# Performance work log

Hardware: AMD Instinct MI355X
Metric: run time of the kernel (lower is better)

## Reference

```python
import jax, jax.numpy as jnp
import numpy as np

IMG = 640.0  # square input image, strides 16/32 -> 40x40 and 20x20 grids

def _decode_level(raw, stride):
    # raw: [B, 5+C, H, W] -> [B, H*W, 5+C] with xy/wh decoded (get_output_and_grid)
    b, ch, h, w = raw.shape
    out = raw.transpose(0, 2, 3, 1).reshape(b, h * w, ch)
    yv, xv = jnp.meshgrid(jnp.arange(h), jnp.arange(w), indexing='ij')
    gx = xv.reshape(-1).astype(raw.dtype)
    gy = yv.reshape(-1).astype(raw.dtype)
    xy = (out[..., :2] + jnp.stack([gx, gy], -1)[None]) * stride
    wh = jnp.exp(out[..., 2:4]) * stride
    out = jnp.concatenate([xy, wh, out[..., 4:]], -1)
    return out, gx, gy, jnp.full((h * w,), stride, raw.dtype)

def _pairwise_iou(a, b):
    # a:[M,4], b:[A,4] in cxcywh -> [M,A] (bboxes_iou, xyxy=False)
    tl = jnp.maximum(a[:, None, :2] - a[:, None, 2:] * 0.5, b[None, :, :2] - b[None, :, 2:] * 0.5)
    br = jnp.minimum(a[:, None, :2] + a[:, None, 2:] * 0.5, b[None, :, :2] + b[None, :, 2:] * 0.5)
    inter = jnp.prod(br - tl, -1) * (tl < br).all(-1)
    area_a = a[:, 2] * a[:, 3]
    area_b = b[:, 2] * b[:, 3]
    return inter / (area_a[:, None] + area_b[None, :] - inter + 1e-16)

def _iou_loss(p, t):
    # YOLOX IOUloss (loss_type='iou'): 1 - iou^2, elementwise over [..., 4] cxcywh
    tl = jnp.maximum(p[..., :2] - p[..., 2:] * 0.5, t[..., :2] - t[..., 2:] * 0.5)
    br = jnp.minimum(p[..., :2] + p[..., 2:] * 0.5, t[..., :2] + t[..., 2:] * 0.5)
    inter = jnp.prod(br - tl, -1) * (tl < br).all(-1)
    iou = inter / (p[..., 2] * p[..., 3] + t[..., 2] * t[..., 3] - inter + 1e-16)
    return 1.0 - iou ** 2

def _bce_logits(x, t):
    # BCEWithLogitsLoss(reduction='none') = softplus(x) - x*t (stable)
    return jnp.logaddexp(0.0, x) - x * t

def _assign_one(bbox_p, cls_p, obj_p, gtb, gtc, gtv, ax, ay, st):
    # SimOTA assignment for one image (mask form of get_assignments, which is @no_grad).
    # bbox_p:[A,4] cls_p:[A,C] obj_p:[A] gtb:[M,4] px cxcywh, gtv:[M] valid mask.
    m = gtb.shape[0]
    axc = (ax + 0.5) * st
    ayc = (ay + 0.5) * st
    gl = gtb[:, 0] - 0.5 * gtb[:, 2]; gr = gtb[:, 0] + 0.5 * gtb[:, 2]
    gtp = gtb[:, 1] - 0.5 * gtb[:, 3]; gbt = gtb[:, 1] + 0.5 * gtb[:, 3]
    in_box = ((axc[None] > gl[:, None]) & (axc[None] < gr[:, None]) &
              (ayc[None] > gtp[:, None]) & (ayc[None] < gbt[:, None])) & gtv[:, None]
    r = 2.5  # center_radius
    in_ctr = ((axc[None] > gtb[:, 0:1] - r * st[None]) & (axc[None] < gtb[:, 0:1] + r * st[None]) &
              (ayc[None] > gtb[:, 1:2] - r * st[None]) & (ayc[None] < gtb[:, 1:2] + r * st[None])) & gtv[:, None]
    fg_cand = (in_box | in_ctr).any(0)          # candidate anchors (fg_mask pre-filter)
    in_both = in_box & in_ctr
    ious = _pairwise_iou(gtb, bbox_p)            # [M,A]
    p = jnp.sqrt(jax.nn.sigmoid(cls_p) * jax.nn.sigmoid(obj_p)[:, None])[None]  # [1,A,C]
    t = jax.nn.one_hot(gtc, cls_p.shape[-1], dtype=p.dtype)[:, None, :]          # [M,1,C]
    eps = 1e-12
    cls_cost = -(t * jnp.log(p + eps) + (1.0 - t) * jnp.log(1.0 - p + eps)).sum(-1)
    invalid = (~fg_cand)[None] | (~gtv)[:, None]
    cost = cls_cost - 3.0 * jnp.log(ious + 1e-8) + 1e5 * (~in_both) + 1e9 * invalid
    ious_m = jnp.where(invalid, 0.0, ious)
    topk, _ = jax.lax.top_k(ious_m, 10)
    dk = jnp.maximum(topk.sum(-1).astype(jnp.int32), 1)  # dynamic_k, clamp min=1
    dk = jnp.where(gtv, dk, 0)
    ranks = jnp.argsort(jnp.argsort(cost, axis=1), axis=1)
    matching = ranks < dk[:, None]                        # top dynamic_k lowest-cost anchors per gt
    conflict = matching.sum(0) > 1
    best_gt = jnp.argmin(cost, 0)
    matching = jnp.where(conflict[None], jnp.arange(m)[:, None] == best_gt[None], matching)
    fg = matching.any(0)
    matched = jnp.argmax(matching, 0).astype(jnp.int32)
    pred_iou = jnp.where(matching, ious, 0.0).sum(0)
    return fg, matched, pred_iou

def _forward(out_l0, out_l1, gt_boxes, gt_classes, num_gts):
    ncls = out_l0.shape[1] - 5
    decs, xs, ys, ss = [], [], [], []
    for raw, stride in ((out_l0, 16.0), (out_l1, 32.0)):
        d, gx, gy, s = _decode_level(raw, stride)
        decs.append(d); xs.append(gx); ys.append(gy); ss.append(s)
    outputs = jnp.concatenate(decs, 1)  # [B, A, 5+C]
    ax = jnp.concatenate(xs); ay = jnp.concatenate(ys); st = jnp.concatenate(ss)
    bbox_p = outputs[..., :4]; obj_p = outputs[..., 4]; cls_p = outputs[..., 5:]
    gtb = gt_boxes * IMG  # normalized -> pixels (imgs_w == imgs_h == IMG)
    gtv = jnp.arange(gt_boxes.shape[1])[None, :] < num_gts[:, None]
    sg = jax.lax.stop_gradient  # get_assignments runs under torch.no_grad
    fg, matched, pred_iou = jax.vmap(_assign_one, in_axes=(0, 0, 0, 0, 0, 0, None, None, None))(
        sg(bbox_p), sg(cls_p), sg(obj_p), sg(gtb), gt_classes, gtv, ax, ay, st)
    fgf = fg.astype(outputs.dtype)
    cls_t = jax.nn.one_hot(jnp.take_along_axis(gt_classes, matched, 1), ncls,
                           dtype=outputs.dtype) * pred_iou[..., None] * fgf[..., None]
    reg_t = jnp.take_along_axis(gtb, matched[..., None], 1)  # [B,A,4]
    num_fg = jnp.maximum(fgf.sum(), 1.0)
    loss_iou = (_iou_loss(bbox_p, reg_t) * fgf).sum() / num_fg
    loss_obj = _bce_logits(obj_p, fgf).sum() / num_fg
    loss_cls = (_bce_logits(cls_p, cls_t) * fgf[..., None]).sum() / num_fg
    total = 5.0 * loss_iou + loss_obj + loss_cls
    return (total, 5.0 * loss_iou, loss_obj, loss_cls,
            num_fg / jnp.maximum(num_gts.sum().astype(outputs.dtype), 1.0))

def setup_inputs() -> dict:
    key = jax.random.key(0)
    k1, k2, k3, k4, k5 = jax.random.split(key, 5)
    return {
        'out_l0': jax.random.normal(k1, (64, 25, 40, 40), jnp.float32),
        'out_l1': jax.random.normal(k2, (64, 25, 20, 20), jnp.float32),
        'gt_boxes': jax.random.uniform(k3, (64, 100, 4), jnp.float32, 1e-3, 1.0),
        'gt_classes': jax.random.randint(k4, (64, 100), 0, 20).astype(jnp.int32),
        'num_gts': jax.random.randint(k5, (64,), 0, 100).astype(jnp.int32),
    }

def reference(out_l0, out_l1, gt_boxes, gt_classes, num_gts):
    return _forward(out_l0, out_l1, gt_boxes, gt_classes, num_gts)
```

## Files before the change

### kernel.cpp

```cpp
#include <hip/hip_runtime.h>
#include <cfloat>
#include <climits>

#define NB 64
#define NA 2000
#define NAP 2048
#define NA0 1600
#define NC 20
#define NM 100

__device__ __forceinline__ void anchor_geom(int a, float& axc, float& ayc, float& st) {
    if (a < NA0) {
        st = 16.0f;
        int x = a % 40, y = a / 40;
        axc = ((float)x + 0.5f) * 16.0f;
        ayc = ((float)y + 0.5f) * 16.0f;
    } else {
        st = 32.0f;
        int aa = a - NA0;
        int x = aa % 20, y = aa / 20;
        axc = ((float)x + 0.5f) * 32.0f;
        ayc = ((float)y + 0.5f) * 32.0f;
    }
}

__device__ __forceinline__ float cost_row(const float4 g, float clsc, const float4 pe, float areaP,
                                          float axc, float ayc, float st, bool fc) {
    float glx = g.x - 0.5f * g.z, grx = g.x + 0.5f * g.z;
    float gty = g.y - 0.5f * g.w, gby = g.y + 0.5f * g.w;
    float tlx = fmaxf(glx, pe.x);
    float tly = fmaxf(gty, pe.z);
    float brx = fminf(grx, pe.y);
    float bry = fminf(gby, pe.w);
    float inter = (brx - tlx) * (bry - tly);
    bool ok = (tlx < brx) && (tly < bry);
    inter = ok ? inter : 0.0f;
    float iou = inter / ((g.z * g.w + areaP) - inter + 1e-16f);
    bool ib = (axc > glx) && (axc < grx) && (ayc > gty) && (ayc < gby);
    bool ic = (axc > g.x - 2.5f * st) && (axc < g.x + 2.5f * st)
           && (ayc > g.y - 2.5f * st) && (ayc < g.y + 2.5f * st);
    return ((clsc - 3.0f * __logf(iou + 1e-8f)) + ((ib && ic) ? 0.0f : 1e5f)) + (fc ? 0.0f : 1e9f);
}

__device__ __forceinline__ unsigned int wave_max_u32(unsigned int x) {
    unsigned int y;
    y = (unsigned)__builtin_amdgcn_update_dpp((int)x, (int)x, 0x111, 0xf, 0xf, false); x = max(x, y);
    y = (unsigned)__builtin_amdgcn_update_dpp((int)x, (int)x, 0x112, 0xf, 0xf, false); x = max(x, y);
    y = (unsigned)__builtin_amdgcn_update_dpp((int)x, (int)x, 0x114, 0xf, 0xf, false); x = max(x, y);
    y = (unsigned)__builtin_amdgcn_update_dpp((int)x, (int)x, 0x118, 0xf, 0xf, false); x = max(x, y);
    y = (unsigned)__builtin_amdgcn_update_dpp((int)x, (int)x, 0x142, 0xa, 0xf, false); x = max(x, y);
    y = (unsigned)__builtin_amdgcn_update_dpp((int)x, (int)x, 0x143, 0xc, 0xf, false); x = max(x, y);
    return (unsigned)__builtin_amdgcn_readlane((int)x, 63);
}
__device__ __forceinline__ unsigned int wave_min_u32(unsigned int x) {
    unsigned int y;
    y = (unsigned)__builtin_amdgcn_update_dpp((int)x, (int)x, 0x111, 0xf, 0xf, false); x = min(x, y);
    y = (unsigned)__builtin_amdgcn_update_dpp((int)x, (int)x, 0x112, 0xf, 0xf, false); x = min(x, y);
    y = (unsigned)__builtin_amdgcn_update_dpp((int)x, (int)x, 0x114, 0xf, 0xf, false); x = min(x, y);
    y = (unsigned)__builtin_amdgcn_update_dpp((int)x, (int)x, 0x118, 0xf, 0xf, false); x = min(x, y);
    y = (unsigned)__builtin_amdgcn_update_dpp((int)x, (int)x, 0x142, 0xa, 0xf, false); x = min(x, y);
    y = (unsigned)__builtin_amdgcn_update_dpp((int)x, (int)x, 0x143, 0xc, 0xf, false); x = min(x, y);
    return (unsigned)__builtin_amdgcn_readlane((int)x, 63);
}

__global__ __launch_bounds__(256) void k_decode(const float* __restrict__ l0, const float* __restrict__ l1,
                                                const float* __restrict__ gt_boxes, const int* __restrict__ num_gts,
                                                float4* __restrict__ ext, float* __restrict__ decA,
                                                float* __restrict__ qq,
                                                unsigned long long* __restrict__ fgw, unsigned int* __restrict__ cm,
                                                float* __restrict__ sp) {
    int b = blockIdx.y;
    int a = blockIdx.x * 256 + threadIdx.x;
    int lane = threadIdx.x & 63;
    __shared__ float4 sext[NM];
    __shared__ float2 sctr[NM];
    __shared__ int sng;
    if (threadIdx.x < NM) {
        float4 g = ((const float4*)gt_boxes)[b * NM + threadIdx.x];
        g.x *= 640.0f; g.y *= 640.0f; g.z *= 640.0f; g.w *= 640.0f;
        sext[threadIdx.x] = make_float4(g.x - 0.5f * g.z, g.x + 0.5f * g.z,
                                        g.y - 0.5f * g.w, g.y + 0.5f * g.w);
        sctr[threadIdx.x] = make_float2(g.x, g.y);
    }
    if (threadIdx.x == 0) sng = num_gts[b];
    __syncthreads();

    size_t pidx = (size_t)b * NAP + a;
    if (a >= NA) {
        cm[pidx] = 0;
        return;
    }

    float v[25];
    if (a < NA0) {
        const float* p = l0 + (size_t)b * 25 * NA0 + a;
#pragma unroll
        for (int c = 0; c < 25; c++) v[c] = p[(size_t)c * NA0];
    } else {
        const float* p = l1 + (size_t)b * 25 * 400 + (a - NA0);
#pragma unroll
        for (int c = 0; c < 25; c++) v[c] = p[(size_t)c * 400];
    }
    float axc, ayc, st;
    anchor_geom(a, axc, ayc, st);
    float gx, gy;
    if (a < NA0) { gx = (float)(a % 40); gy = (float)(a / 40); }
    else { int aa = a - NA0; gx = (float)(aa % 20); gy = (float)(aa / 20); }
    float4 pb;
    pb.x = (v[0] + gx) * st;
    pb.y = (v[1] + gy) * st;
    pb.z = expf(v[2]) * st;
    pb.w = expf(v[3]) * st;
    ext[pidx] = make_float4(pb.x - 0.5f * pb.z, pb.x + 0.5f * pb.z,
                            pb.y - 0.5f * pb.w, pb.y + 0.5f * pb.w);
    decA[pidx] = pb.z * pb.w;

    float sob = 1.0f / (1.0f + __expf(-v[4]));
    float d[NC];
    float s = 0.0f;
    float spv = 0.0f;
#pragma unroll
    for (int c = 0; c < NC; c++) {
        float x = v[5 + c];
        float sc = 1.0f / (1.0f + __expf(-x));
        float p = sqrtf(sc * sob);
        float lp = __logf(p + 1e-12f);
        float lq = __logf(1.0f - p + 1e-12f);
        s += -lq;
        d[c] = lq - lp;
        spv += fmaxf(x, 0.0f) + log1pf(__expf(-fabsf(x)));
    }
#pragma unroll
    for (int c = 0; c < NC; c++)
        qq[((size_t)b * NC + c) * NAP + a] = s + d[c];
    sp[pidx] = spv;

    int ng = sng;
    int f = 0;
    float rst = 2.5f * st;
    for (int m = 0; m < ng; m++) {
        float4 e = sext[m];
        float2 cc = sctr[m];
        bool ib = (axc > e.x) && (axc < e.y) && (ayc > e.z) && (ayc < e.w);
        bool ic = (axc > cc.x - rst) && (axc < cc.x + rst) && (ayc > cc.y - rst) && (ayc < cc.y + rst);
        if (ib || ic) { f = 1; break; }
    }
    unsigned long long mk = __ballot(f);
    if (lane == 0) fgw[(size_t)b * 32 + (a >> 6)] = mk;
    cm[pidx] = 0;
}

__global__ __launch_bounds__(256) void k_assign(const float* __restrict__ gt_boxes, const int* __restrict__ gt_classes,
                                                const int* __restrict__ num_gts, const float4* __restrict__ ext,
                                                const float* __restrict__ decA,
                                                const float* __restrict__ qq, const unsigned long long* __restrict__ fgw,
                                                unsigned int* __restrict__ cm) {
    int lane = threadIdx.x & 63;
    int wv = __builtin_amdgcn_readfirstlane((int)(threadIdx.x >> 6));
    int rloc = wv >> 1, half = wv & 1;
    int row = __builtin_amdgcn_readfirstlane((int)(blockIdx.x * 2 + rloc));
    int b = row / NM, m = row - b * NM;
    bool valid = (m < num_gts[b]);

    __shared__ unsigned int lA[2][2][10];
    __shared__ unsigned int lB[2][2][10];
    __shared__ unsigned int lmeta[2];
    __shared__ unsigned int lthr[2];

    unsigned int ik[16], ck[16];
    size_t bNA = (size_t)b * NAP;
    unsigned int inc = (1u << 20) + (unsigned)m;

    if (valid) {
        float4 g = ((const float4*)gt_boxes)[b * NM + m];
        g.x *= 640.0f; g.y *= 640.0f; g.z *= 640.0f; g.w *= 640.0f;
        int tc = gt_classes[b * NM + m];
        const float* qrow = qq + ((size_t)b * NC + tc) * NAP;

        float glx = g.x - 0.5f * g.z, grx = g.x + 0.5f * g.z;
        float gty = g.y - 0.5f * g.w, gby = g.y + 0.5f * g.w;
        float areag = g.z * g.w;
        float c16l = g.x - 40.0f, c16r = g.x + 40.0f, c16t = g.y - 40.0f, c16b = g.y + 40.0f;
        float c32l = g.x - 80.0f, c32r = g.x + 80.0f, c32t = g.y - 80.0f, c32b = g.y + 80.0f;

#pragma unroll
        for (int j = 0; j < 16; j++) {
            int jj = half * 16 + j;
            int a = jj * 64 + lane;
            bool lvl0 = jj < 25;
            float stj = lvl0 ? 16.0f : 32.0f;
            int rel = lvl0 ? a : (a - NA0);
            int W = lvl0 ? 40 : 20;
            int gyv = rel / W;
            int gxv = rel - gyv * W;
            float axc = ((float)gxv + 0.5f) * stj;
            float ayc = ((float)gyv + 0.5f) * stj;
            unsigned long long fw = fgw[(size_t)b * 32 + jj];
            bool fc = (fw >> lane) & 1ULL;
            float4 pe = ext[bNA + a];
            float areaP = decA[bNA + a];
            float clsc = qrow[a];
            float tlx = fmaxf(glx, pe.x);
            float tly = fmaxf(gty, pe.z);
            float brx = fminf(grx, pe.y);
            float bry = fminf(gby, pe.w);
            float inter = (brx - tlx) * (bry - tly);
            bool ok = (tlx < brx) && (tly < bry);
            inter = ok ? inter : 0.0f;
            float iou = inter / ((areag + areaP) - inter + 1e-16f);
            bool ib = (axc > glx) && (axc < grx) && (ayc > gty) && (ayc < gby);
            bool ic = lvl0 ? ((axc > c16l) && (axc < c16r) && (ayc > c16t) && (ayc < c16b))
                           : ((axc > c32l) && (axc < c32r) && (ayc > c32t) && (ayc < c32b));
            float cc = ((clsc - 3.0f * __logf(iou + 1e-8f)) + ((ib && ic) ? 0.0f : 1e5f)) + (fc ? 0.0f : 1e9f);
            float im = fc ? iou : 0.0f;
            ik[j] = (__float_as_uint(im) & 0xFFFFF800u) | (unsigned)a;
            ck[j] = (__float_as_uint(cc) & 0xFFFFF800u) | (unsigned)a;
        }

        int k = 0;
#pragma unroll 1
        for (; k < 10; ++k) {
            unsigned int t[8];
#pragma unroll
            for (int h = 0; h < 8; h++) t[h] = max(ik[2 * h], ik[2 * h + 1]);
#pragma unroll
            for (int w = 4; w >= 1; w >>= 1)
#pragma unroll
                for (int h = 0; h < w; h++) t[h] = max(t[h], t[h + w]);
            unsigned int mx = wave_max_u32(t[0]);
            if ((mx & 0xFFFFF800u) == 0u) break;
            if (lane == 0) lA[rloc][half][k] = mx;
#pragma unroll
            for (int j = 0; j < 16; j++) ik[j] = (ik[j] == mx) ? 0u : ik[j];
        }
#pragma unroll 1
        for (; k < 10; ++k) if (lane == 0) lA[rloc][half][k] = 0u;
    }
    __syncthreads();

    if (valid && half == 0 && lane == 0) {
        int i0 = 0, i1 = 0;
        float s = 0.0f;
        for (int k = 0; k < 10; k++) {
            unsigned int a0 = lA[rloc][0][i0], a1 = lA[rloc][1][i1];
            unsigned int mx;
            if (a1 > a0) { mx = a1; i1++; } else { mx = a0; i0++; }
            s += __uint_as_float(mx & 0xFFFFF800u);
        }
        int dk = (int)s;
        if (dk < 1) dk = 1;
        lmeta[rloc] = (unsigned)dk;
    }
    __syncthreads();

    int dkv = 0;
    if (valid) dkv = __builtin_amdgcn_readfirstlane((int)lmeta[rloc]);

    if (valid) {
#pragma unroll 1
        for (int k = 0; k < dkv; k++) {
            unsigned int t[8];
#pragma unroll
            for (int h = 0; h < 8; h++) t[h] = min(ck[2 * h], ck[2 * h + 1]);
#pragma unroll
            for (int w = 4; w >= 1; w >>= 1)
#pragma unroll
                for (int h = 0; h < w; h++) t[h] = min(t[h], t[h + w]);
            unsigned int mn = wave_min_u32(t[0]);
            if (lane == 0) lB[rloc][half][k] = mn;
#pragma unroll
            for (int j = 0; j < 16; j++) ck[j] = (ck[j] == mn) ? 0xFFFFFFFFu : ck[j];
        }
    }
    __syncthreads();

    if (valid && half == 0 && lane == 0) {
        int i0 = 0, i1 = 0;
        unsigned int thr = 0;
        for (int k = 0; k < dkv; k++) {
            unsigned int a0 = lB[rloc][0][i0], a1 = lB[rloc][1][i1];
            if (a1 < a0) { thr = a1; i1++; } else { thr = a0; i0++; }
        }
        lthr[rloc] = thr;
    }
    __syncthreads();

    if (valid) {
        unsigned int thr = (unsigned)__builtin_amdgcn_readfirstlane((int)lthr[rloc]);
        unsigned int mb = 0;
#pragma unroll
        for (int j = 0; j < 16; j++) if (ck[j] <= thr) mb |= 1u << j;
#pragma unroll 1
        for (int k = 0; k < dkv; k++) {
            unsigned int e = lB[rloc][half][k];
            if (e <= thr) {
                unsigned int idx = e & 0x7FFu;
                if ((int)(idx & 63u) == lane) mb |= 1u << ((int)(idx >> 6) - half * 16);
            }
        }
#pragma unroll
        for (int j = 0; j < 16; j++) {
            if ((mb >> j) & 1u) atomicAdd(&cm[bNA + (size_t)(half * 16 + j) * 64 + lane], inc);
        }
    }
}

__global__ __launch_bounds__(256) void k_resolve(const float* __restrict__ l0, const float* __restrict__ l1,
                                                 const float* __restrict__ gt_boxes, const int* __restrict__ gt_classes,
                                                 const int* __restrict__ num_gts,
                                                 const float4* __restrict__ ext, const float* __restrict__ decA,
                                                 const float* __restrict__ qq, const unsigned long long* __restrict__ fgw,
                                                 const unsigned int* __restrict__ cm,
                                                 const float* __restrict__ sp,
                                                 float* __restrict__ partials) {
    int gtid = blockIdx.x * 256 + threadIdx.x;
    int lane = threadIdx.x & 63;
    int b = gtid >> 11;
    int a = gtid & (NAP - 1);
    bool real = a < NA;

    unsigned int word = real ? cm[gtid] : 0u;
    int mres = (int)(word & 0xFFFFFu);

    unsigned long long msk = __ballot((word >> 20) >= 2u);
    if (msk != 0ull) {
        int base = gtid & ~63;
        int ng = num_gts[b];
        while (msk) {
            int t = __ffsll((long long)msk) - 1;
            msk &= msk - 1;
            int idx = base + t;
            int aa = idx & (NAP - 1);
            float4 pe = ext[idx];
            float areaP = decA[idx];
            float axc, ayc, st;
            anchor_geom(aa, axc, ayc, st);
            bool fcq = (fgw[(size_t)b * 32 + (aa >> 6)] >> (aa & 63)) & 1ULL;
            unsigned int best = 0xFFFFFFFFu;
#pragma unroll
            for (int half = 0; half < 2; half++) {
                int m = half * 64 + lane;
                if (m < ng) {
                    float4 g = ((const float4*)gt_boxes)[b * NM + m];
                    g.x *= 640.0f; g.y *= 640.0f; g.z *= 640.0f; g.w *= 640.0f;
                    int tcm = gt_classes[b * NM + m];
                    float clsc = qq[((size_t)b * NC + tcm) * NAP + aa];
                    float cc = cost_row(g, clsc, pe, areaP, axc, ayc, st, fcq);
                    unsigned int key = (__float_as_uint(cc) & 0xFFFFF800u) | (unsigned)m;
                    best = min(best, key);
                }
            }
#pragma unroll
            for (int o = 1; o < 64; o <<= 1) {
                unsigned int ov = (unsigned int)__shfl_xor((int)best, o);
                best = min(best, ov);
            }
            if (lane == t) mres = (int)(best & 0x7FFu);
        }
    }

    float lobj = 0.0f, liou = 0.0f, lcls = 0.0f, fgf = 0.0f;
    if (real) {
        float objv;
        if (a < NA0) objv = l0[((size_t)b * 25 + 4) * NA0 + a];
        else         objv = l1[((size_t)b * 25 + 4) * 400 + (a - NA0)];
        bool fg = (word >> 20) > 0;
        fgf = fg ? 1.0f : 0.0f;
        lobj = (fmaxf(objv, 0.0f) + log1pf(expf(-fabsf(objv)))) - objv * fgf;
        if (fg) {
            float4 pe = ext[gtid];
            float areaP = decA[gtid];
            int m = mres;
            float4 g = ((const float4*)gt_boxes)[b * NM + m];
            g.x *= 640.0f; g.y *= 640.0f; g.z *= 640.0f; g.w *= 640.0f;
            float tlx = fmaxf(pe.x, g.x - 0.5f * g.z);
            float tly = fmaxf(pe.z, g.y - 0.5f * g.w);
            float brx = fminf(pe.y, g.x + 0.5f * g.z);
            float bry = fminf(pe.w, g.y + 0.5f * g.w);
            float inter = (brx - tlx) * (bry - tly);
            bool ok = (tlx < brx) && (tly < bry);
            inter = ok ? inter : 0.0f;
            float iou = inter / ((areaP + g.z * g.w) - inter + 1e-16f);
            liou = 1.0f - iou * iou;
            float piou = iou;
            int tcm = gt_classes[b * NM + m];
            float x_t;
            if (a < NA0) x_t = l0[((size_t)b * 25 + 5 + tcm) * NA0 + a];
            else         x_t = l1[((size_t)b * 25 + 5 + tcm) * 400 + (a - NA0)];
            lcls = sp[gtid] - x_t * piou;
        }
    }

    __shared__ float s0[256], s1[256], s2[256], s3[256];
    int t = threadIdx.x;
    s0[t] = lobj; s1[t] = liou; s2[t] = lcls; s3[t] = fgf;
    __syncthreads();
    for (int o = 128; o > 0; o >>= 1) {
        if (t < o) { s0[t] += s0[t + o]; s1[t] += s1[t + o]; s2[t] += s2[t + o]; s3[t] += s3[t + o]; }
        __syncthreads();
    }
    if (t == 0) {
        partials[blockIdx.x * 4 + 0] = s0[0];
        partials[blockIdx.x * 4 + 1] = s1[0];
        partials[blockIdx.x * 4 + 2] = s2[0];
        partials[blockIdx.x * 4 + 3] = s3[0];
    }
}

__global__ __launch_bounds__(256) void k_final(const float* __restrict__ partials, int nblocks,
                                               const int* __restrict__ num_gts, float* __restrict__ out) {
    __shared__ float s0[256], s1[256], s2[256], s3[256];
    int t = threadIdx.x;
    float a0 = 0, a1 = 0, a2 = 0, a3 = 0;
    for (int i = t; i < nblocks; i += 256) {
        a0 += partials[i * 4 + 0];
        a1 += partials[i * 4 + 1];
        a2 += partials[i * 4 + 2];
        a3 += partials[i * 4 + 3];
    }
    s0[t] = a0; s1[t] = a1; s2[t] = a2; s3[t] = a3;
    __syncthreads();
    for (int o = 128; o > 0; o >>= 1) {
        if (t < o) { s0[t] += s0[t + o]; s1[t] += s1[t + o]; s2[t] += s2[t + o]; s3[t] += s3[t + o]; }
        __syncthreads();
    }
    if (t == 0) {
        int sg = 0;
        for (int i = 0; i < NB; i++) sg += num_gts[i];
        float num_fg = fmaxf(s3[0], 1.0f);
        float li5 = 5.0f * (s1[0] / num_fg);
        float lo = s0[0] / num_fg;
        float lcx = s2[0] / num_fg;
        out[0] = li5 + lo + lcx;
        out[1] = li5;
        out[2] = lo;
        out[3] = lcx;
        out[4] = num_fg / fmaxf((float)sg, 1.0f);
    }
}

extern "C" void kernel_launch(void* const* d_in, const int* in_sizes, int n_in,
                              void* d_out, int out_size, void* d_ws, size_t ws_size,
                              hipStream_t stream) {
    const float* l0 = (const float*)d_in[0];
    const float* l1 = (const float*)d_in[1];
    const float* gt_boxes = (const float*)d_in[2];
    const int* gt_classes = (const int*)d_in[3];
    const int* num_gts = (const int*)d_in[4];
    float* out = (float*)d_out;

    char* w = (char*)d_ws;
    float4* ext  = (float4*)(w);
    float* decA  = (float*)(w + 2097152);
    float* qq    = (float*)(w + 2621440);
    unsigned long long* fgw = (unsigned long long*)(w + 13107200);
    unsigned int* cm = (unsigned int*)(w + 13123584);
    float* sp    = (float*)(w + 13647872);
    float* partials = (float*)(w + 14172160);

    (void)n_in; (void)in_sizes; (void)out_size; (void)ws_size;

    k_decode<<<dim3(8, NB), 256, 0, stream>>>(l0, l1, gt_boxes, num_gts, ext, decA, qq, fgw, cm, sp);
    k_assign<<<(NB * NM) / 2, 256, 0, stream>>>(gt_boxes, gt_classes, num_gts, ext, decA, qq, fgw, cm);
    k_resolve<<<(NB * NAP) / 256, 256, 0, stream>>>(l0, l1, gt_boxes, gt_classes, num_gts, ext, decA, qq, fgw, cm, sp, partials);
    k_final<<<1, 256, 0, stream>>>(partials, (NB * NAP) / 256, num_gts, out);
}
```

Before: 73.02 us.

## Split each GT row across four waves and fuse final reduction into resolve

The assign kernel now gives each GT row a full 256-thread block of four waves, each holding 8 anchors' keys instead of 16, and merges the per-wave top-k lists four ways. Blocks for invalid GT rows return early. The separate final-reduction kernel is removed: the last block of the resolve kernel, found with an atomic ticket counter that the decode kernel resets, sums the partials and writes the losses. This trades shorter per-wave serial selection loops and one fewer launch for more blocks, a serial four-way merge, and atomic and fence overhead.

```diff
diff --git a/kernel.cpp b/kernel.cpp
--- a/kernel.cpp
+++ b/kernel.cpp
@@ -68,7 +68,7 @@
                                                 float4* __restrict__ ext, float* __restrict__ decA,
                                                 float* __restrict__ qq,
                                                 unsigned long long* __restrict__ fgw, unsigned int* __restrict__ cm,
-                                                float* __restrict__ sp) {
+                                                float* __restrict__ sp, unsigned int* __restrict__ counter) {
     int b = blockIdx.y;
     int a = blockIdx.x * 256 + threadIdx.x;
     int lane = threadIdx.x & 63;
@@ -83,6 +83,7 @@
         sctr[threadIdx.x] = make_float2(g.x, g.y);
     }
     if (threadIdx.x == 0) sng = num_gts[b];
+    if (b == 0 && blockIdx.x == 0 && threadIdx.x == 0) *counter = 0u;
     __syncthreads();
 
     size_t pidx = (size_t)b * NAP + a;
@@ -157,21 +158,20 @@
                                                 unsigned int* __restrict__ cm) {
     int lane = threadIdx.x & 63;
     int wv = __builtin_amdgcn_readfirstlane((int)(threadIdx.x >> 6));
-    int rloc = wv >> 1, half = wv & 1;
-    int row = __builtin_amdgcn_readfirstlane((int)(blockIdx.x * 2 + rloc));
+    int row = __builtin_amdgcn_readfirstlane((int)blockIdx.x);
     int b = row / NM, m = row - b * NM;
-    bool valid = (m < num_gts[b]);
-
-    __shared__ unsigned int lA[2][2][10];
-    __shared__ unsigned int lB[2][2][10];
-    __shared__ unsigned int lmeta[2];
-    __shared__ unsigned int lthr[2];
-
-    unsigned int ik[16], ck[16];
+    if (m >= num_gts[b]) return;
+
+    __shared__ unsigned int lA[4][10];
+    __shared__ unsigned int lB[4][10];
+    __shared__ unsigned int lmeta;
+    __shared__ unsigned int lthr;
+
+    unsigned int ik[8], ck[8];
     size_t bNA = (size_t)b * NAP;
     unsigned int inc = (1u << 20) + (unsigned)m;
 
-    if (valid) {
+    {
         float4 g = ((const float4*)gt_boxes)[b * NM + m];
         g.x *= 640.0f; g.y *= 640.0f; g.z *= 640.0f; g.w *= 640.0f;
         int tc = gt_classes[b * NM + m];
@@ -184,15 +184,16 @@
         float c32l = g.x - 80.0f, c32r = g.x + 80.0f, c32t = g.y - 80.0f, c32b = g.y + 80.0f;
 
 #pragma unroll
-        for (int j = 0; j < 16; j++) {
-            int jj = half * 16 + j;
+        for (int j = 0; j < 8; j++) {
+            int jj = wv * 8 + j;
             int a = jj * 64 + lane;
             bool lvl0 = jj < 25;
             float stj = lvl0 ? 16.0f : 32.0f;
-            int rel = lvl0 ? a : (a - NA0);
-            int W = lvl0 ? 40 : 20;
-            int gyv = rel / W;
-            int gxv = rel - gyv * W;
+            int y40 = a / 40;
+            int aa2 = a - NA0;
+            int y20 = aa2 / 20;
+            int gyv = lvl0 ? y40 : y20;
+            int gxv = lvl0 ? (a - y40 * 40) : (aa2 - y20 * 20);
             float axc = ((float)gxv + 0.5f) * stj;
             float ayc = ((float)gyv + 0.5f) * stj;
             unsigned long long fw = fgw[(size_t)b * 32 + jj];
@@ -216,91 +217,86 @@
             ik[j] = (__float_as_uint(im) & 0xFFFFF800u) | (unsigned)a;
             ck[j] = (__float_as_uint(cc) & 0xFFFFF800u) | (unsigned)a;
         }
-
+    }
+
+    {
         int k = 0;
 #pragma unroll 1
         for (; k < 10; ++k) {
-            unsigned int t[8];
-#pragma unroll
-            for (int h = 0; h < 8; h++) t[h] = max(ik[2 * h], ik[2 * h + 1]);
-#pragma unroll
-            for (int w = 4; w >= 1; w >>= 1)
-#pragma unroll
-                for (int h = 0; h < w; h++) t[h] = max(t[h], t[h + w]);
+            unsigned int t[4];
+#pragma unroll
+            for (int h = 0; h < 4; h++) t[h] = max(ik[2 * h], ik[2 * h + 1]);
+            t[0] = max(t[0], t[2]); t[1] = max(t[1], t[3]); t[0] = max(t[0], t[1]);
             unsigned int mx = wave_max_u32(t[0]);
             if ((mx & 0xFFFFF800u) == 0u) break;
-            if (lane == 0) lA[rloc][half][k] = mx;
-#pragma unroll
-            for (int j = 0; j < 16; j++) ik[j] = (ik[j] == mx) ? 0u : ik[j];
+            if (lane == 0) lA[wv][k] = mx;
+#pragma unroll
+            for (int j = 0; j < 8; j++) ik[j] = (ik[j] == mx) ? 0u : ik[j];
         }
 #pragma unroll 1
-        for (; k < 10; ++k) if (lane == 0) lA[rloc][half][k] = 0u;
-    }
-    __syncthreads();
-
-    if (valid && half == 0 && lane == 0) {
-        int i0 = 0, i1 = 0;
+        for (; k < 10; ++k) if (lane == 0) lA[wv][k] = 0u;
+    }
+    __syncthreads();
+
+    if (threadIdx.x == 0) {
+        int i0 = 0, i1 = 0, i2 = 0, i3 = 0;
         float s = 0.0f;
         for (int k = 0; k < 10; k++) {
-            unsigned int a0 = lA[rloc][0][i0], a1 = lA[rloc][1][i1];
-            unsigned int mx;
-            if (a1 > a0) { mx = a1; i1++; } else { mx = a0; i0++; }
+            unsigned int a0 = lA[0][i0], a1 = lA[1][i1], a2 = lA[2][i2], a3 = lA[3][i3];
+            unsigned int mx = max(max(a0, a1), max(a2, a3));
+            if (mx == a0) i0++; else if (mx == a1) i1++; else if (mx == a2) i2++; else i3++;
             s += __uint_as_float(mx & 0xFFFFF800u);
         }
         int dk = (int)s;
         if (dk < 1) dk = 1;
-        lmeta[rloc] = (unsigned)dk;
-    }
-    __syncthreads();
-
-    int dkv = 0;
-    if (valid) dkv = __builtin_amdgcn_readfirstlane((int)lmeta[rloc]);
-
-    if (valid) {
+        lmeta = (unsigned)dk;
+    }
+    __syncthreads();
+
+    int dkv = __builtin_amdgcn_readfirstlane((int)lmeta);
+
+#pragma unroll 1
+    for (int k = 0; k < dkv; k++) {
+        unsigned int t[4];
+#pragma unroll
+        for (int h = 0; h < 4; h++) t[h] = min(ck[2 * h], ck[2 * h + 1]);
+        t[0] = min(t[0], t[2]); t[1] = min(t[1], t[3]); t[0] = min(t[0], t[1]);
+        unsigned int mn = wave_min_u32(t[0]);
+        if (lane == 0) lB[wv][k] = mn;
+#pragma unroll
+        for (int j = 0; j < 8; j++) ck[j] = (ck[j] == mn) ? 0xFFFFFFFFu : ck[j];
+    }
+    __syncthreads();
+
+    if (threadIdx.x == 0) {
+        int i0 = 0, i1 = 0, i2 = 0, i3 = 0;
+        unsigned int thr = 0;
+        for (int k = 0; k < dkv; k++) {
+            unsigned int a0 = lB[0][i0], a1 = lB[1][i1], a2 = lB[2][i2], a3 = lB[3][i3];
+            unsigned int mn = min(min(a0, a1), min(a2, a3));
+            if (mn == a0) i0++; else if (mn == a1) i1++; else if (mn == a2) i2++; else i3++;
+            thr = mn;
+        }
+        lthr = thr;
+    }
+    __syncthreads();
+
+    {
+        unsigned int thr = (unsigned)__builtin_amdgcn_readfirstlane((int)lthr);
+        unsigned int mb = 0;
+#pragma unroll
+        for (int j = 0; j < 8; j++) if (ck[j] <= thr) mb |= 1u << j;
 #pragma unroll 1
         for (int k = 0; k < dkv; k++) {
-            unsigned int t[8];
-#pragma unroll
-            for (int h = 0; h < 8; h++) t[h] = min(ck[2 * h], ck[2 * h + 1]);
-#pragma unroll
-            for (int w = 4; w >= 1; w >>= 1)
-#pragma unroll
-                for (int h = 0; h < w; h++) t[h] = min(t[h], t[h + w]);
-            unsigned int mn = wave_min_u32(t[0]);
-            if (lane == 0) lB[rloc][half][k] = mn;
-#pragma unroll
-            for (int j = 0; j < 16; j++) ck[j] = (ck[j] == mn) ? 0xFFFFFFFFu : ck[j];
-        }
-    }
-    __syncthreads();
-
-    if (valid && half == 0 && lane == 0) {
-        int i0 = 0, i1 = 0;
-        unsigned int thr = 0;
-        for (int k = 0; k < dkv; k++) {
-            unsigned int a0 = lB[rloc][0][i0], a1 = lB[rloc][1][i1];
-            if (a1 < a0) { thr = a1; i1++; } else { thr = a0; i0++; }
-        }
-        lthr[rloc] = thr;
-    }
-    __syncthreads();
-
-    if (valid) {
-        unsigned int thr = (unsigned)__builtin_amdgcn_readfirstlane((int)lthr[rloc]);
-        unsigned int mb = 0;
-#pragma unroll
-        for (int j = 0; j < 16; j++) if (ck[j] <= thr) mb |= 1u << j;
-#pragma unroll 1
-        for (int k = 0; k < dkv; k++) {
-            unsigned int e = lB[rloc][half][k];
+            unsigned int e = lB[wv][k];
             if (e <= thr) {
                 unsigned int idx = e & 0x7FFu;
-                if ((int)(idx & 63u) == lane) mb |= 1u << ((int)(idx >> 6) - half * 16);
+                if ((int)(idx & 63u) == lane) mb |= 1u << ((int)(idx >> 6) - wv * 8);
             }
         }
 #pragma unroll
-        for (int j = 0; j < 16; j++) {
-            if ((mb >> j) & 1u) atomicAdd(&cm[bNA + (size_t)(half * 16 + j) * 64 + lane], inc);
+        for (int j = 0; j < 8; j++) {
+            if ((mb >> j) & 1u) atomicAdd(&cm[bNA + (size_t)(wv * 8 + j) * 64 + lane], inc);
         }
     }
 }
@@ -312,7 +308,8 @@
                                                  const float* __restrict__ qq, const unsigned long long* __restrict__ fgw,
                                                  const unsigned int* __restrict__ cm,
                                                  const float* __restrict__ sp,
-                                                 float* __restrict__ partials) {
+                                                 float* __restrict__ partials, unsigned int* __restrict__ counter,
+                                                 float* __restrict__ out) {
     int gtid = blockIdx.x * 256 + threadIdx.x;
     int lane = threadIdx.x & 63;
     int b = gtid >> 11;
@@ -405,37 +402,41 @@
         partials[blockIdx.x * 4 + 2] = s2[0];
         partials[blockIdx.x * 4 + 3] = s3[0];
     }
-}
-
-__global__ __launch_bounds__(256) void k_final(const float* __restrict__ partials, int nblocks,
-                                               const int* __restrict__ num_gts, float* __restrict__ out) {
-    __shared__ float s0[256], s1[256], s2[256], s3[256];
-    int t = threadIdx.x;
-    float a0 = 0, a1 = 0, a2 = 0, a3 = 0;
-    for (int i = t; i < nblocks; i += 256) {
-        a0 += partials[i * 4 + 0];
-        a1 += partials[i * 4 + 1];
-        a2 += partials[i * 4 + 2];
-        a3 += partials[i * 4 + 3];
-    }
-    s0[t] = a0; s1[t] = a1; s2[t] = a2; s3[t] = a3;
-    __syncthreads();
-    for (int o = 128; o > 0; o >>= 1) {
-        if (t < o) { s0[t] += s0[t + o]; s1[t] += s1[t + o]; s2[t] += s2[t + o]; s3[t] += s3[t + o]; }
+
+    __threadfence();
+    __shared__ unsigned int sticket;
+    if (t == 0) sticket = atomicAdd(counter, 1u);
+    __syncthreads();
+    if (sticket == (unsigned)(gridDim.x - 1)) {
+        __threadfence();
+        const volatile float* vp = partials;
+        float a0 = 0, a1 = 0, a2 = 0, a3 = 0;
+        int nblocks = (int)gridDim.x;
+        for (int i = t; i < nblocks; i += 256) {
+            a0 += vp[i * 4 + 0];
+            a1 += vp[i * 4 + 1];
+            a2 += vp[i * 4 + 2];
+            a3 += vp[i * 4 + 3];
+        }
+        s0[t] = a0; s1[t] = a1; s2[t] = a2; s3[t] = a3;
         __syncthreads();
-    }
-    if (t == 0) {
-        int sg = 0;
-        for (int i = 0; i < NB; i++) sg += num_gts[i];
-        float num_fg = fmaxf(s3[0], 1.0f);
-        float li5 = 5.0f * (s1[0] / num_fg);
-        float lo = s0[0] / num_fg;
-        float lcx = s2[0] / num_fg;
-        out[0] = li5 + lo + lcx;
-        out[1] = li5;
-        out[2] = lo;
-        out[3] = lcx;
-        out[4] = num_fg / fmaxf((float)sg, 1.0f);
+        for (int o = 128; o > 0; o >>= 1) {
+            if (t < o) { s0[t] += s0[t + o]; s1[t] += s1[t + o]; s2[t] += s2[t + o]; s3[t] += s3[t + o]; }
+            __syncthreads();
+        }
+        if (t == 0) {
+            int sg = 0;
+            for (int i = 0; i < NB; i++) sg += num_gts[i];
+            float num_fg = fmaxf(s3[0], 1.0f);
+            float li5 = 5.0f * (s1[0] / num_fg);
+            float lo = s0[0] / num_fg;
+            float lcx = s2[0] / num_fg;
+            out[0] = li5 + lo + lcx;
+            out[1] = li5;
+            out[2] = lo;
+            out[3] = lcx;
+            out[4] = num_fg / fmaxf((float)sg, 1.0f);
+        }
     }
 }
 
@@ -457,11 +458,11 @@
     unsigned int* cm = (unsigned int*)(w + 13123584);
     float* sp    = (float*)(w + 13647872);
     float* partials = (float*)(w + 14172160);
+    unsigned int* counter = (unsigned int*)(w + 14180352);
 
     (void)n_in; (void)in_sizes; (void)out_size; (void)ws_size;
 
-    k_decode<<<dim3(8, NB), 256, 0, stream>>>(l0, l1, gt_boxes, num_gts, ext, decA, qq, fgw, cm, sp);
-    k_assign<<<(NB * NM) / 2, 256, 0, stream>>>(gt_boxes, gt_classes, num_gts, ext, decA, qq, fgw, cm);
-    k_resolve<<<(NB * NAP) / 256, 256, 0, stream>>>(l0, l1, gt_boxes, gt_classes, num_gts, ext, decA, qq, fgw, cm, sp, partials);
-    k_final<<<1, 256, 0, stream>>>(partials, (NB * NAP) / 256, num_gts, out);
-}
+    k_decode<<<dim3(8, NB), 256, 0, stream>>>(l0, l1, gt_boxes, num_gts, ext, decA, qq, fgw, cm, sp, counter);
+    k_assign<<<NB * NM, 256, 0, stream>>>(gt_boxes, gt_classes, num_gts, ext, decA, qq, fgw, cm);
+    k_resolve<<<(NB * NAP) / 256, 256, 0, stream>>>(l0, l1, gt_boxes, gt_classes, num_gts, ext, decA, qq, fgw, cm, sp, partials, counter, out);
+}
```

After: 113.9 us. 56.0% more time.
